# Optimization experiments

Hardware: AMD Instinct MI355X
Metric: run time of the kernel (lower is better)

## Reference

```python
import jax, jax.numpy as jnp
import numpy as np

B, T_EN, T_DE, D_EN, D_DE, UNITS = 8, 512, 128, 512, 512, 256


def setup_inputs() -> dict:
    key = jax.random.key(0)
    k1, k2, k3, k4, k5, k6 = jax.random.split(key, 6)
    return {
        "en_seq": jax.random.normal(k1, (B, T_EN, D_EN), dtype=jnp.float32),
        "de_seq": jax.random.normal(k2, (B, T_DE, D_DE), dtype=jnp.float32),
        "mask_en": jax.random.randint(k3, (B, T_EN), 0, 2, dtype=jnp.int32),
        "w_en": jax.random.normal(k4, (D_EN, UNITS), dtype=jnp.float32) * (1.0 / np.sqrt(D_EN)),
        "w_de": jax.random.normal(k5, (D_DE, UNITS), dtype=jnp.float32) * (1.0 / np.sqrt(D_DE)),
        "nu": jax.random.normal(k6, (UNITS, 1), dtype=jnp.float32) * (1.0 / np.sqrt(UNITS)),
    }


def reference(en_seq, de_seq, mask_en, w_en, w_de, nu):
    # Additive (Bahdanau) attention scores.
    att_en = jnp.einsum('bed,du->beu', en_seq, w_en)   # [B, T_en, U]
    att_de = jnp.einsum('btd,du->btu', de_seq, w_de)   # [B, T_de, U]
    # co_m[b, j, i, u] = att_de[b, j, u] + att_en[b, i, u]
    co_m = jnp.tanh(att_de[:, :, None, :] + att_en[:, None, :, :])  # [B, T_de, T_en, U]
    mu = jnp.einsum('btiu,uo->bti', co_m, nu)          # [B, T_de, T_en]
    # mask: (m - 1) * 1e6 added to logits (m in {0,1})
    m = mask_en.astype(mu.dtype)                       # [B, T_en]
    mu = mu + ((m - 1.0) * 1000000.0)[:, None, :]
    return jax.nn.softmax(mu, axis=-1)                 # [B, T_de, T_en]
```

## Files before the change

### kernel.cpp

```cpp
#include <hip/hip_runtime.h>
#include <cstddef>
#include <cstdint>

#define B_    8
#define T_EN_ 512
#define T_DE_ 128
#define D_    512
#define U_    256

#define TANH_C 2.8853900817779268f
#define L2E_   1.4426950408889634f

typedef float f32x4 __attribute__((ext_vector_type(4)));
typedef float f32x2 __attribute__((ext_vector_type(2)));
typedef short s16x8 __attribute__((ext_vector_type(8)));

__device__ __forceinline__ float exp2c(float x) {
  return __builtin_amdgcn_exp2f(x * TANH_C);
}

__device__ __forceinline__ void split_bf16(float x, short& hi, short& lo) {
  const unsigned u = __float_as_uint(x);
  hi = (short)(u >> 16);
  const float hf = __uint_as_float(u & 0xffff0000u);
  const float lf = x - hf;
  lo = (short)(__float_as_uint(lf) >> 16);
}

__global__ __launch_bounds__(256) void prepack_kernel(
    const float* __restrict__ en, const float* __restrict__ de,
    const float* __restrict__ w_en, const float* __restrict__ w_de,
    short* __restrict__ en_hi, short* __restrict__ en_lo,
    short* __restrict__ de_hi, short* __restrict__ de_lo,
    short* __restrict__ wen_hi, short* __restrict__ wen_lo,
    short* __restrict__ wde_hi, short* __restrict__ wde_lo) {
  const int blk = blockIdx.x;
  const int tid = threadIdx.x;
  float v[8];
  short* ph;
  short* pl;
  size_t ub;

  if (blk < 1280) {
    const int gu = blk * 256 + tid;
    const int n = gu & 15;
    const int g = (gu >> 4) & 3;
    const int s = (gu >> 6) & 15;
    const int rb = gu >> 10;
    const float* src;
    if (rb < 256) {
      const int b = rb >> 5, t = rb & 31;
      src = en + ((size_t)rb * 16 + n) * D_;
      ub = ((size_t)((b * 16 + s) * 32 + t) * 4 + g) * 16 + n;
      ph = en_hi; pl = en_lo;
    } else {
      const int t64 = rb - 256;
      src = de + ((size_t)t64 * 16 + n) * D_;
      ub = ((size_t)(s * 64 + t64) * 4 + g) * 16 + n;
      ph = de_hi; pl = de_lo;
    }
    const int kb = s * 32 + g * 4;
    const float4 fa = *(const float4*)(src + kb);
    const float4 fb = *(const float4*)(src + kb + 16);
    v[0] = fa.x; v[1] = fa.y; v[2] = fa.z; v[3] = fa.w;
    v[4] = fb.x; v[5] = fb.y; v[6] = fb.z; v[7] = fb.w;
  } else {
    const int wb = blk - 1280;
    const bool is_en = wb < 64;
    const int wq = wb & 63;
    const int s = wq >> 2, USq = wq & 3;
    const int n = tid & 15;
    const int g = (tid >> 4) & 3;
    const int US = USq * 4 + (tid >> 6);
    const float* W = is_en ? w_en : w_de;
    ph = is_en ? wen_hi : wde_hi;
    pl = is_en ? wen_lo : wde_lo;
    #pragma unroll
    for (int e = 0; e < 8; ++e) {
      const int k = s * 32 + g * 4 + (e & 3) + 16 * (e >> 2);
      v[e] = W[(size_t)k * U_ + US * 16 + n];
    }
    ub = ((size_t)(s * 16 + US) * 4 + g) * 16 + n;
  }

  s16x8 h8, l8;
  #pragma unroll
  for (int e = 0; e < 8; ++e) {
    short h, l;
    split_bf16(v[e], h, l);
    h8[e] = h; l8[e] = l;
  }
  *(s16x8*)(ph + ub * 8) = h8;
  *(s16x8*)(pl + ub * 8) = l8;
}

__global__ __launch_bounds__(256) void mfma_proj_kernel(
    const short* __restrict__ en_hi, const short* __restrict__ en_lo,
    const short* __restrict__ de_hi, const short* __restrict__ de_lo,
    const short* __restrict__ wen_hi, const short* __restrict__ wen_lo,
    const short* __restrict__ wde_hi, const short* __restrict__ wde_lo,
    float* __restrict__ Et, float* __restrict__ de_t) {
  const int blk = blockIdx.x;
  const int tid = threadIdx.x;
  const int lane = tid & 63;
  const int wv = tid >> 6;
  const int rl = lane >> 4, cl = lane & 15;

  f32x4 acc[2] = {};
  s16x8 bufA[6], bufB[6];

  if (blk < 512) {
    const int b  = blk & 7;
    const int uh = (blk >> 3) & 1;
    const int it = blk >> 4;
    const int US0 = uh * 8 + wv * 2;

#define LOAD_EN(DST, S)                                                   \
    { const size_t oa0 = ((size_t)((S) * 16 + US0) * 64 + lane) * 8;      \
      const size_t ob  = ((size_t)((b * 16 + (S)) * 32 + it) * 64 + lane) * 8; \
      DST[0] = *(const s16x8*)(wen_hi + oa0);                             \
      DST[1] = *(const s16x8*)(wen_lo + oa0);                             \
      DST[2] = *(const s16x8*)(wen_hi + oa0 + 512);                       \
      DST[3] = *(const s16x8*)(wen_lo + oa0 + 512);                       \
      DST[4] = *(const s16x8*)(en_hi + ob);                               \
      DST[5] = *(const s16x8*)(en_lo + ob); }
#define MFMA_EN(S)                                                        \
    { acc[0] = __builtin_amdgcn_mfma_f32_16x16x32_bf16(S[0], S[4], acc[0], 0, 0, 0); \
      acc[0] = __builtin_amdgcn_mfma_f32_16x16x32_bf16(S[0], S[5], acc[0], 0, 0, 0); \
      acc[0] = __builtin_amdgcn_mfma_f32_16x16x32_bf16(S[1], S[4], acc[0], 0, 0, 0); \
      acc[1] = __builtin_amdgcn_mfma_f32_16x16x32_bf16(S[2], S[4], acc[1], 0, 0, 0); \
      acc[1] = __builtin_amdgcn_mfma_f32_16x16x32_bf16(S[2], S[5], acc[1], 0, 0, 0); \
      acc[1] = __builtin_amdgcn_mfma_f32_16x16x32_bf16(S[3], S[4], acc[1], 0, 0, 0); }

    LOAD_EN(bufA, 0)
    for (int s = 0; s < 16; s += 2) {
      LOAD_EN(bufB, s + 1)
      MFMA_EN(bufA)
      if (s + 2 < 16) LOAD_EN(bufA, s + 2)
      MFMA_EN(bufB)
    }
#undef LOAD_EN
#undef MFMA_EN

    #pragma unroll
    for (int us = 0; us < 2; ++us) {
      #pragma unroll
      for (int r = 0; r < 4; ++r) {
        const int u = (US0 + us) * 16 + rl * 4 + r;
        const int i = it * 16 + cl;
        Et[((size_t)b * U_ + u) * T_EN_ + i] = exp2c(acc[us][r]);
      }
    }
  } else {
    const int y = blk - 512;
    const int t64 = y >> 1;
    const int uh = y & 1;
    const int US0 = uh * 8 + wv * 2;

#define LOAD_DE(DST, S)                                                   \
    { const size_t oa = ((size_t)((S) * 64 + t64) * 64 + lane) * 8;       \
      const size_t ob = ((size_t)((S) * 16 + US0) * 64 + lane) * 8;       \
      DST[0] = *(const s16x8*)(de_hi + oa);                               \
      DST[1] = *(const s16x8*)(de_lo + oa);                               \
      DST[2] = *(const s16x8*)(wde_hi + ob);                              \
      DST[3] = *(const s16x8*)(wde_lo + ob);                              \
      DST[4] = *(const s16x8*)(wde_hi + ob + 512);                        \
      DST[5] = *(const s16x8*)(wde_lo + ob + 512); }
#define MFMA_DE(S)                                                        \
    { acc[0] = __builtin_amdgcn_mfma_f32_16x16x32_bf16(S[0], S[2], acc[0], 0, 0, 0); \
      acc[0] = __builtin_amdgcn_mfma_f32_16x16x32_bf16(S[0], S[3], acc[0], 0, 0, 0); \
      acc[0] = __builtin_amdgcn_mfma_f32_16x16x32_bf16(S[1], S[2], acc[0], 0, 0, 0); \
      acc[1] = __builtin_amdgcn_mfma_f32_16x16x32_bf16(S[0], S[4], acc[1], 0, 0, 0); \
      acc[1] = __builtin_amdgcn_mfma_f32_16x16x32_bf16(S[0], S[5], acc[1], 0, 0, 0); \
      acc[1] = __builtin_amdgcn_mfma_f32_16x16x32_bf16(S[1], S[4], acc[1], 0, 0, 0); }

    LOAD_DE(bufA, 0)
    for (int s = 0; s < 16; s += 2) {
      LOAD_DE(bufB, s + 1)
      MFMA_DE(bufA)
      if (s + 2 < 16) LOAD_DE(bufA, s + 2)
      MFMA_DE(bufB)
    }
#undef LOAD_DE
#undef MFMA_DE

    #pragma unroll
    for (int us = 0; us < 2; ++us) {
      #pragma unroll
      for (int r = 0; r < 4; ++r) {
        const int j = t64 * 16 + rl * 4 + r;
        const int u = (US0 + us) * 16 + cl;
        de_t[(size_t)j * U_ + u] = exp2c(acc[us][r]);
      }
    }
  }
}

__global__ __launch_bounds__(512) void attn_mu_softmax_kernel(
    const float* __restrict__ Et, const float* __restrict__ de_t,
    const float* __restrict__ nu, const int* __restrict__ mask,
    float* __restrict__ out) {
  __shared__ f32x2 Ea_s[4][U_ / 2];
  __shared__ f32x2 nv2_s[U_ / 2];
  __shared__ float mu_p[8][4][T_EN_];

  const int tid  = threadIdx.x;
  const int lane = tid & 63;
  const int w    = tid >> 6;
  const int b    = blockIdx.x & 7;
  const int jg   = blockIdx.x >> 3;
  const int j0   = jg * 4;

  {
    const int jl = tid >> 7;
    const int p  = tid & 127;
    const float2 Av = *(const float2*)(de_t + (size_t)(b * T_DE_ + j0 + jl) * U_ + 2 * p);
    f32x2 L; L[0] = Av.x; L[1] = Av.y;
    Ea_s[jl][p] = L;
    if (tid < 128) {
      const float2 n2 = *(const float2*)(nu + 2 * tid);
      f32x2 v; v[0] = n2.x; v[1] = n2.y;
      nv2_s[tid] = v;
    }
  }
  __syncthreads();

  const int pb = w * 16;
  const float* __restrict__ EbA =
      Et + ((size_t)b * U_ + 2 * pb) * T_EN_ + lane * 4;

  const f32x4 one4 = {1.f, 1.f, 1.f, 1.f};
  f32x4 accA[4] = {}, accB[4] = {};

  f32x4 E1Aa, E1Ba, E2Aa, E2Ba, E1Ab, E1Bb, E2Ab, E2Bb;
  f32x2 La[4], Lb[4];
  f32x2 nva, nvb;

#define LOADP(SUF, P)                                                     \
  { const float* e1 = EbA + (size_t)(2 * (P)) * T_EN_;                    \
    const float* e2 = e1 + T_EN_;                                         \
    E1A##SUF = *(const f32x4*)(e1);                                       \
    E1B##SUF = *(const f32x4*)(e1 + 256);                                 \
    E2A##SUF = *(const f32x4*)(e2);                                       \
    E2B##SUF = *(const f32x4*)(e2 + 256);                                 \
    L##SUF[0] = Ea_s[0][pb + (P)];                                        \
    L##SUF[1] = Ea_s[1][pb + (P)];                                        \
    L##SUF[2] = Ea_s[2][pb + (P)];                                        \
    L##SUF[3] = Ea_s[3][pb + (P)];                                        \
    nv##SUF = nv2_s[pb + (P)]; }

#define COMPP(SUF)                                                        \
  { _Pragma("unroll")                                                     \
    for (int jl = 0; jl < 4; ++jl) {                                      \
      const f32x2 Lc = L##SUF[jl];                                        \
      { const f32x4 d1 = E1A##SUF * Lc[0] + one4;                         \
        const f32x4 d2 = E2A##SUF * Lc[1] + one4;                         \
        const f32x4 t  = d2 * nv##SUF[0];                                 \
        const f32x4 num = d1 * nv##SUF[1] + t;                            \
        const f32x4 Dd = d1 * d2;                                         \
        f32x4 r;                                                          \
        r[0] = __builtin_amdgcn_rcpf(Dd[0]);                              \
        r[1] = __builtin_amdgcn_rcpf(Dd[1]);                              \
        r[2] = __builtin_amdgcn_rcpf(Dd[2]);                              \
        r[3] = __builtin_amdgcn_rcpf(Dd[3]);                              \
        accA[jl] = num * r + accA[jl]; }                                  \
      { const f32x4 d1 = E1B##SUF * Lc[0] + one4;                         \
        const f32x4 d2 = E2B##SUF * Lc[1] + one4;                         \
        const f32x4 t  = d2 * nv##SUF[0];                                 \
        const f32x4 num = d1 * nv##SUF[1] + t;                            \
        const f32x4 Dd = d1 * d2;                                         \
        f32x4 r;                                                          \
        r[0] = __builtin_amdgcn_rcpf(Dd[0]);                              \
        r[1] = __builtin_amdgcn_rcpf(Dd[1]);                              \
        r[2] = __builtin_amdgcn_rcpf(Dd[2]);                              \
        r[3] = __builtin_amdgcn_rcpf(Dd[3]);                              \
        accB[jl] = num * r + accB[jl]; }                                  \
    } }

  LOADP(a, 0)
  for (int p0 = 0; p0 < 16; p0 += 2) {
    LOADP(b, p0 + 1)
    COMPP(a)
    if (p0 + 2 < 16) LOADP(a, p0 + 2)
    COMPP(b)
  }
#undef LOADP
#undef COMPP

  #pragma unroll
  for (int jl = 0; jl < 4; ++jl) {
    *(f32x4*)&mu_p[w][jl][lane * 4] = accA[jl];
    *(f32x4*)&mu_p[w][jl][256 + lane * 4] = accB[jl];
  }
  __syncthreads();

  if (w < 4) {
    float vals[8];
    float mx = -3.0e38f;
    #pragma unroll
    for (int h = 0; h < 2; ++h) {
      f32x4 s = {0.f, 0.f, 0.f, 0.f};
      #pragma unroll
      for (int uo = 0; uo < 8; ++uo)
        s += *(const f32x4*)&mu_p[uo][w][h * 256 + lane * 4];
      const int4 mk = *(const int4*)(mask + b * T_EN_ + h * 256 + lane * 4);
      const float v0 = fmaf((float)mk.x - 1.f, 1.0e6f, -2.f * s[0]);
      const float v1 = fmaf((float)mk.y - 1.f, 1.0e6f, -2.f * s[1]);
      const float v2 = fmaf((float)mk.z - 1.f, 1.0e6f, -2.f * s[2]);
      const float v3 = fmaf((float)mk.w - 1.f, 1.0e6f, -2.f * s[3]);
      vals[h * 4 + 0] = v0; vals[h * 4 + 1] = v1;
      vals[h * 4 + 2] = v2; vals[h * 4 + 3] = v3;
      mx = fmaxf(mx, fmaxf(fmaxf(v0, v1), fmaxf(v2, v3)));
    }
    #pragma unroll
    for (int off = 32; off; off >>= 1) mx = fmaxf(mx, __shfl_xor(mx, off, 64));
    float sum = 0.0f;
    #pragma unroll
    for (int k = 0; k < 8; ++k) {
      const float e = __builtin_amdgcn_exp2f((vals[k] - mx) * L2E_);
      vals[k] = e;
      sum += e;
    }
    #pragma unroll
    for (int off = 32; off; off >>= 1) sum += __shfl_xor(sum, off, 64);
    const float inv = __builtin_amdgcn_rcpf(sum);
    float* op = out + (size_t)(b * T_DE_ + j0 + w) * T_EN_;
    #pragma unroll
    for (int h = 0; h < 2; ++h) {
      const float4 o = make_float4(vals[h * 4 + 0] * inv, vals[h * 4 + 1] * inv,
                                   vals[h * 4 + 2] * inv, vals[h * 4 + 3] * inv);
      *(float4*)(op + h * 256 + lane * 4) = o;
    }
  }
}

extern "C" void kernel_launch(void* const* d_in, const int* in_sizes, int n_in,
                              void* d_out, int out_size, void* d_ws, size_t ws_size,
                              hipStream_t stream) {
  const float* en   = (const float*)d_in[0];
  const float* de   = (const float*)d_in[1];
  const int*   mask = (const int*)d_in[2];
  const float* w_en = (const float*)d_in[3];
  const float* w_de = (const float*)d_in[4];
  const float* nu   = (const float*)d_in[5];
  float* out = (float*)d_out;

  float* Et   = (float*)d_ws;
  float* de_t = Et + (size_t)B_ * U_ * T_EN_;
  short* p    = (short*)(de_t + (size_t)B_ * T_DE_ * U_);
  short* en_hi = p;                 p += 2097152;
  short* en_lo = p;                 p += 2097152;
  short* de_hi = p;                 p += 524288;
  short* de_lo = p;                 p += 524288;
  short* wen_hi = p;                p += 131072;
  short* wen_lo = p;                p += 131072;
  short* wde_hi = p;                p += 131072;
  short* wde_lo = p;                p += 131072;

  prepack_kernel<<<dim3(1408), 256, 0, stream>>>(
      en, de, w_en, w_de, en_hi, en_lo, de_hi, de_lo,
      wen_hi, wen_lo, wde_hi, wde_lo);
  mfma_proj_kernel<<<dim3(640), 256, 0, stream>>>(
      en_hi, en_lo, de_hi, de_lo, wen_hi, wen_lo, wde_hi, wde_lo, Et, de_t);
  attn_mu_softmax_kernel<<<dim3(256), 512, 0, stream>>>(
      Et, de_t, nu, mask, out);
}
```

Before: 39.00 us.

## Retile encoder projection and attention kernel; split softmax into separate kernel

The encoder projection now computes two 16-wide i-tiles per wave, reusing each weight fragment across both and halving that part of the grid. The attention kernel now handles 8 decoder rows over half of T_en per block instead of 4 rows over all of T_en, so each Et load is reused across more rows. Because a block no longer sees a full row, softmax moves to a new kernel that reads mu from a workspace buffer. This adds a launch and a global round trip for mu, in exchange for more register-level reuse and better load balance.

```diff
diff --git a/kernel.cpp b/kernel.cpp
--- a/kernel.cpp
+++ b/kernel.cpp
@@ -106,31 +106,39 @@
   const int wv = tid >> 6;
   const int rl = lane >> 4, cl = lane & 15;
 
-  f32x4 acc[2] = {};
-  s16x8 bufA[6], bufB[6];
-
-  if (blk < 512) {
+  if (blk < 256) {
     const int b  = blk & 7;
     const int uh = (blk >> 3) & 1;
     const int it = blk >> 4;
     const int US0 = uh * 8 + wv * 2;
 
+    f32x4 acc[2][2] = {};
+    s16x8 bufA[8], bufB[8];
+
 #define LOAD_EN(DST, S)                                                   \
     { const size_t oa0 = ((size_t)((S) * 16 + US0) * 64 + lane) * 8;      \
-      const size_t ob  = ((size_t)((b * 16 + (S)) * 32 + it) * 64 + lane) * 8; \
+      const size_t ob0 = ((size_t)(((b * 16 + (S)) * 32 + it * 2)) * 64 + lane) * 8; \
       DST[0] = *(const s16x8*)(wen_hi + oa0);                             \
       DST[1] = *(const s16x8*)(wen_lo + oa0);                             \
       DST[2] = *(const s16x8*)(wen_hi + oa0 + 512);                       \
       DST[3] = *(const s16x8*)(wen_lo + oa0 + 512);                       \
-      DST[4] = *(const s16x8*)(en_hi + ob);                               \
-      DST[5] = *(const s16x8*)(en_lo + ob); }
+      DST[4] = *(const s16x8*)(en_hi + ob0);                              \
+      DST[5] = *(const s16x8*)(en_lo + ob0);                              \
+      DST[6] = *(const s16x8*)(en_hi + ob0 + 512);                        \
+      DST[7] = *(const s16x8*)(en_lo + ob0 + 512); }
 #define MFMA_EN(S)                                                        \
-    { acc[0] = __builtin_amdgcn_mfma_f32_16x16x32_bf16(S[0], S[4], acc[0], 0, 0, 0); \
-      acc[0] = __builtin_amdgcn_mfma_f32_16x16x32_bf16(S[0], S[5], acc[0], 0, 0, 0); \
-      acc[0] = __builtin_amdgcn_mfma_f32_16x16x32_bf16(S[1], S[4], acc[0], 0, 0, 0); \
-      acc[1] = __builtin_amdgcn_mfma_f32_16x16x32_bf16(S[2], S[4], acc[1], 0, 0, 0); \
-      acc[1] = __builtin_amdgcn_mfma_f32_16x16x32_bf16(S[2], S[5], acc[1], 0, 0, 0); \
-      acc[1] = __builtin_amdgcn_mfma_f32_16x16x32_bf16(S[3], S[4], acc[1], 0, 0, 0); }
+    { acc[0][0] = __builtin_amdgcn_mfma_f32_16x16x32_bf16(S[0], S[4], acc[0][0], 0, 0, 0); \
+      acc[0][0] = __builtin_amdgcn_mfma_f32_16x16x32_bf16(S[0], S[5], acc[0][0], 0, 0, 0); \
+      acc[0][0] = __builtin_amdgcn_mfma_f32_16x16x32_bf16(S[1], S[4], acc[0][0], 0, 0, 0); \
+      acc[0][1] = __builtin_amdgcn_mfma_f32_16x16x32_bf16(S[0], S[6], acc[0][1], 0, 0, 0); \
+      acc[0][1] = __builtin_amdgcn_mfma_f32_16x16x32_bf16(S[0], S[7], acc[0][1], 0, 0, 0); \
+      acc[0][1] = __builtin_amdgcn_mfma_f32_16x16x32_bf16(S[1], S[6], acc[0][1], 0, 0, 0); \
+      acc[1][0] = __builtin_amdgcn_mfma_f32_16x16x32_bf16(S[2], S[4], acc[1][0], 0, 0, 0); \
+      acc[1][0] = __builtin_amdgcn_mfma_f32_16x16x32_bf16(S[2], S[5], acc[1][0], 0, 0, 0); \
+      acc[1][0] = __builtin_amdgcn_mfma_f32_16x16x32_bf16(S[3], S[4], acc[1][0], 0, 0, 0); \
+      acc[1][1] = __builtin_amdgcn_mfma_f32_16x16x32_bf16(S[2], S[6], acc[1][1], 0, 0, 0); \
+      acc[1][1] = __builtin_amdgcn_mfma_f32_16x16x32_bf16(S[2], S[7], acc[1][1], 0, 0, 0); \
+      acc[1][1] = __builtin_amdgcn_mfma_f32_16x16x32_bf16(S[3], S[6], acc[1][1], 0, 0, 0); }
 
     LOAD_EN(bufA, 0)
     for (int s = 0; s < 16; s += 2) {
@@ -145,17 +153,23 @@
     #pragma unroll
     for (int us = 0; us < 2; ++us) {
       #pragma unroll
-      for (int r = 0; r < 4; ++r) {
-        const int u = (US0 + us) * 16 + rl * 4 + r;
-        const int i = it * 16 + cl;
-        Et[((size_t)b * U_ + u) * T_EN_ + i] = exp2c(acc[us][r]);
+      for (int is = 0; is < 2; ++is) {
+        #pragma unroll
+        for (int r = 0; r < 4; ++r) {
+          const int u = (US0 + us) * 16 + rl * 4 + r;
+          const int i = it * 32 + is * 16 + cl;
+          Et[((size_t)b * U_ + u) * T_EN_ + i] = exp2c(acc[us][is][r]);
+        }
       }
     }
   } else {
-    const int y = blk - 512;
+    const int y = blk - 256;
     const int t64 = y >> 1;
     const int uh = y & 1;
     const int US0 = uh * 8 + wv * 2;
+
+    f32x4 acc[2] = {};
+    s16x8 bufA[6], bufB[6];
 
 #define LOAD_DE(DST, S)                                                   \
     { const size_t oa = ((size_t)((S) * 64 + t64) * 64 + lane) * 8;       \
@@ -196,85 +210,71 @@
   }
 }
 
-__global__ __launch_bounds__(512) void attn_mu_softmax_kernel(
+__global__ __launch_bounds__(512) void attn_mu_kernel(
     const float* __restrict__ Et, const float* __restrict__ de_t,
-    const float* __restrict__ nu, const int* __restrict__ mask,
-    float* __restrict__ out) {
-  __shared__ f32x2 Ea_s[4][U_ / 2];
+    const float* __restrict__ nu, float* __restrict__ mu) {
+  __shared__ f32x2 Ea_s[8][U_ / 2];
   __shared__ f32x2 nv2_s[U_ / 2];
-  __shared__ float mu_p[8][4][T_EN_];
+  __shared__ float mu_p[8][8][256];
 
   const int tid  = threadIdx.x;
   const int lane = tid & 63;
   const int w    = tid >> 6;
   const int b    = blockIdx.x & 7;
-  const int jg   = blockIdx.x >> 3;
-  const int j0   = jg * 4;
-
-  {
-    const int jl = tid >> 7;
-    const int p  = tid & 127;
+  const int ih   = (blockIdx.x >> 3) & 1;
+  const int jo   = blockIdx.x >> 4;
+  const int j0   = jo * 8;
+
+  #pragma unroll
+  for (int e0 = 0; e0 < 2; ++e0) {
+    const int e = tid + e0 * 512;
+    const int jl = e >> 7;
+    const int p  = e & 127;
     const float2 Av = *(const float2*)(de_t + (size_t)(b * T_DE_ + j0 + jl) * U_ + 2 * p);
     f32x2 L; L[0] = Av.x; L[1] = Av.y;
     Ea_s[jl][p] = L;
-    if (tid < 128) {
-      const float2 n2 = *(const float2*)(nu + 2 * tid);
-      f32x2 v; v[0] = n2.x; v[1] = n2.y;
-      nv2_s[tid] = v;
-    }
+  }
+  if (tid < 128) {
+    const float2 n2 = *(const float2*)(nu + 2 * tid);
+    f32x2 v; v[0] = n2.x; v[1] = n2.y;
+    nv2_s[tid] = v;
   }
   __syncthreads();
 
   const int pb = w * 16;
-  const float* __restrict__ EbA =
-      Et + ((size_t)b * U_ + 2 * pb) * T_EN_ + lane * 4;
+  const float* __restrict__ Eb =
+      Et + ((size_t)b * U_ + 2 * pb) * T_EN_ + ih * 256 + lane * 4;
 
   const f32x4 one4 = {1.f, 1.f, 1.f, 1.f};
-  f32x4 accA[4] = {}, accB[4] = {};
-
-  f32x4 E1Aa, E1Ba, E2Aa, E2Ba, E1Ab, E1Bb, E2Ab, E2Bb;
-  f32x2 La[4], Lb[4];
+  f32x4 acc[8] = {};
+
+  f32x4 E1a, E2a, E1b, E2b;
+  f32x2 La[8], Lb[8];
   f32x2 nva, nvb;
 
 #define LOADP(SUF, P)                                                     \
-  { const float* e1 = EbA + (size_t)(2 * (P)) * T_EN_;                    \
-    const float* e2 = e1 + T_EN_;                                         \
-    E1A##SUF = *(const f32x4*)(e1);                                       \
-    E1B##SUF = *(const f32x4*)(e1 + 256);                                 \
-    E2A##SUF = *(const f32x4*)(e2);                                       \
-    E2B##SUF = *(const f32x4*)(e2 + 256);                                 \
-    L##SUF[0] = Ea_s[0][pb + (P)];                                        \
-    L##SUF[1] = Ea_s[1][pb + (P)];                                        \
-    L##SUF[2] = Ea_s[2][pb + (P)];                                        \
-    L##SUF[3] = Ea_s[3][pb + (P)];                                        \
+  { const float* e1 = Eb + (size_t)(2 * (P)) * T_EN_;                     \
+    E1##SUF = *(const f32x4*)(e1);                                        \
+    E2##SUF = *(const f32x4*)(e1 + T_EN_);                                \
+    _Pragma("unroll")                                                     \
+    for (int jl = 0; jl < 8; ++jl) L##SUF[jl] = Ea_s[jl][pb + (P)];       \
     nv##SUF = nv2_s[pb + (P)]; }
 
 #define COMPP(SUF)                                                        \
   { _Pragma("unroll")                                                     \
-    for (int jl = 0; jl < 4; ++jl) {                                      \
+    for (int jl = 0; jl < 8; ++jl) {                                      \
       const f32x2 Lc = L##SUF[jl];                                        \
-      { const f32x4 d1 = E1A##SUF * Lc[0] + one4;                         \
-        const f32x4 d2 = E2A##SUF * Lc[1] + one4;                         \
-        const f32x4 t  = d2 * nv##SUF[0];                                 \
-        const f32x4 num = d1 * nv##SUF[1] + t;                            \
-        const f32x4 Dd = d1 * d2;                                         \
-        f32x4 r;                                                          \
-        r[0] = __builtin_amdgcn_rcpf(Dd[0]);                              \
-        r[1] = __builtin_amdgcn_rcpf(Dd[1]);                              \
-        r[2] = __builtin_amdgcn_rcpf(Dd[2]);                              \
-        r[3] = __builtin_amdgcn_rcpf(Dd[3]);                              \
-        accA[jl] = num * r + accA[jl]; }                                  \
-      { const f32x4 d1 = E1B##SUF * Lc[0] + one4;                         \
-        const f32x4 d2 = E2B##SUF * Lc[1] + one4;                         \
-        const f32x4 t  = d2 * nv##SUF[0];                                 \
-        const f32x4 num = d1 * nv##SUF[1] + t;                            \
-        const f32x4 Dd = d1 * d2;                                         \
-        f32x4 r;                                                          \
-        r[0] = __builtin_amdgcn_rcpf(Dd[0]);                              \
-        r[1] = __builtin_amdgcn_rcpf(Dd[1]);                              \
-        r[2] = __builtin_amdgcn_rcpf(Dd[2]);                              \
-        r[3] = __builtin_amdgcn_rcpf(Dd[3]);                              \
-        accB[jl] = num * r + accB[jl]; }                                  \
+      const f32x4 d1 = E1##SUF * Lc[0] + one4;                            \
+      const f32x4 d2 = E2##SUF * Lc[1] + one4;                            \
+      const f32x4 t  = d2 * nv##SUF[0];                                   \
+      const f32x4 num = d1 * nv##SUF[1] + t;                              \
+      const f32x4 Dd = d1 * d2;                                           \
+      f32x4 r;                                                            \
+      r[0] = __builtin_amdgcn_rcpf(Dd[0]);                                \
+      r[1] = __builtin_amdgcn_rcpf(Dd[1]);                                \
+      r[2] = __builtin_amdgcn_rcpf(Dd[2]);                                \
+      r[3] = __builtin_amdgcn_rcpf(Dd[3]);                                \
+      acc[jl] = num * r + acc[jl];                                        \
     } }
 
   LOADP(a, 0)
@@ -288,50 +288,54 @@
 #undef COMPP
 
   #pragma unroll
-  for (int jl = 0; jl < 4; ++jl) {
-    *(f32x4*)&mu_p[w][jl][lane * 4] = accA[jl];
-    *(f32x4*)&mu_p[w][jl][256 + lane * 4] = accB[jl];
-  }
+  for (int jl = 0; jl < 8; ++jl)
+    *(f32x4*)&mu_p[w][jl][lane * 4] = acc[jl];
   __syncthreads();
 
-  if (w < 4) {
-    float vals[8];
-    float mx = -3.0e38f;
+  {
+    f32x4 s = {0.f, 0.f, 0.f, 0.f};
     #pragma unroll
-    for (int h = 0; h < 2; ++h) {
-      f32x4 s = {0.f, 0.f, 0.f, 0.f};
-      #pragma unroll
-      for (int uo = 0; uo < 8; ++uo)
-        s += *(const f32x4*)&mu_p[uo][w][h * 256 + lane * 4];
-      const int4 mk = *(const int4*)(mask + b * T_EN_ + h * 256 + lane * 4);
-      const float v0 = fmaf((float)mk.x - 1.f, 1.0e6f, -2.f * s[0]);
-      const float v1 = fmaf((float)mk.y - 1.f, 1.0e6f, -2.f * s[1]);
-      const float v2 = fmaf((float)mk.z - 1.f, 1.0e6f, -2.f * s[2]);
-      const float v3 = fmaf((float)mk.w - 1.f, 1.0e6f, -2.f * s[3]);
-      vals[h * 4 + 0] = v0; vals[h * 4 + 1] = v1;
-      vals[h * 4 + 2] = v2; vals[h * 4 + 3] = v3;
-      mx = fmaxf(mx, fmaxf(fmaxf(v0, v1), fmaxf(v2, v3)));
-    }
-    #pragma unroll
-    for (int off = 32; off; off >>= 1) mx = fmaxf(mx, __shfl_xor(mx, off, 64));
-    float sum = 0.0f;
-    #pragma unroll
-    for (int k = 0; k < 8; ++k) {
-      const float e = __builtin_amdgcn_exp2f((vals[k] - mx) * L2E_);
-      vals[k] = e;
-      sum += e;
-    }
-    #pragma unroll
-    for (int off = 32; off; off >>= 1) sum += __shfl_xor(sum, off, 64);
-    const float inv = __builtin_amdgcn_rcpf(sum);
-    float* op = out + (size_t)(b * T_DE_ + j0 + w) * T_EN_;
-    #pragma unroll
-    for (int h = 0; h < 2; ++h) {
-      const float4 o = make_float4(vals[h * 4 + 0] * inv, vals[h * 4 + 1] * inv,
-                                   vals[h * 4 + 2] * inv, vals[h * 4 + 3] * inv);
-      *(float4*)(op + h * 256 + lane * 4) = o;
-    }
-  }
+    for (int uo = 0; uo < 8; ++uo)
+      s += *(const f32x4*)&mu_p[uo][w][lane * 4];
+    const f32x4 o = s * -2.0f;
+    *(f32x4*)(mu + (size_t)(b * T_DE_ + j0 + w) * T_EN_ + ih * 256 + lane * 4) = o;
+  }
+}
+
+__global__ __launch_bounds__(512) void softmax_kernel(
+    const float* __restrict__ mu, const int* __restrict__ mask,
+    float* __restrict__ out) {
+  const int tid  = threadIdx.x;
+  const int lane = tid & 63;
+  const int jd   = blockIdx.x * 8 + (tid >> 6);
+  const int b    = jd >> 7;
+
+  const float* mp = mu + (size_t)jd * T_EN_;
+  float vals[8];
+  float mx = -3.0e38f;
+  #pragma unroll
+  for (int k = 0; k < 8; ++k) {
+    const int i = lane + 64 * k;
+    const float mi = (float)mask[b * T_EN_ + i];
+    const float v = fmaf(mi - 1.0f, 1.0e6f, mp[i]);
+    vals[k] = v;
+    mx = fmaxf(mx, v);
+  }
+  #pragma unroll
+  for (int off = 32; off; off >>= 1) mx = fmaxf(mx, __shfl_xor(mx, off, 64));
+  float sum = 0.0f;
+  #pragma unroll
+  for (int k = 0; k < 8; ++k) {
+    const float e = __builtin_amdgcn_exp2f((vals[k] - mx) * L2E_);
+    vals[k] = e;
+    sum += e;
+  }
+  #pragma unroll
+  for (int off = 32; off; off >>= 1) sum += __shfl_xor(sum, off, 64);
+  const float inv = __builtin_amdgcn_rcpf(sum);
+  float* op = out + (size_t)jd * T_EN_;
+  #pragma unroll
+  for (int k = 0; k < 8; ++k) op[lane + 64 * k] = vals[k] * inv;
 }
 
 extern "C" void kernel_launch(void* const* d_in, const int* in_sizes, int n_in,
@@ -347,7 +351,8 @@
 
   float* Et   = (float*)d_ws;
   float* de_t = Et + (size_t)B_ * U_ * T_EN_;
-  short* p    = (short*)(de_t + (size_t)B_ * T_DE_ * U_);
+  float* muB  = de_t + (size_t)B_ * T_DE_ * U_;
+  short* p    = (short*)(muB + (size_t)B_ * T_DE_ * T_EN_);
   short* en_hi = p;                 p += 2097152;
   short* en_lo = p;                 p += 2097152;
   short* de_hi = p;                 p += 524288;
@@ -360,8 +365,8 @@
   prepack_kernel<<<dim3(1408), 256, 0, stream>>>(
       en, de, w_en, w_de, en_hi, en_lo, de_hi, de_lo,
       wen_hi, wen_lo, wde_hi, wde_lo);
-  mfma_proj_kernel<<<dim3(640), 256, 0, stream>>>(
+  mfma_proj_kernel<<<dim3(384), 256, 0, stream>>>(
       en_hi, en_lo, de_hi, de_lo, wen_hi, wen_lo, wde_hi, wde_lo, Et, de_t);
-  attn_mu_softmax_kernel<<<dim3(256), 512, 0, stream>>>(
-      Et, de_t, nu, mask, out);
-}
+  attn_mu_kernel<<<dim3(256), 512, 0, stream>>>(Et, de_t, nu, muB);
+  softmax_kernel<<<dim3(128), 512, 0, stream>>>(muB, mask, out);
+}
```

Result: slower. 41.11 us (+5.4%).

## Deepen projection load prefetch and halve decoder rows per attention block

Applied to the files above, without the earlier changes.

The projection kernel now keeps four stages of register buffers in flight instead of two, aiming to hide more global load latency behind the MFMAs. The attention kernel handles 2 decoder rows per block instead of 4, doubling the grid to 512 blocks, shrinking shared memory, and adding a min-blocks hint to raise occupancy. The trade-off is that each Et tile loaded from global memory is now reused across fewer decoder rows, doubling Et traffic. The extra prefetch buffers also raise register pressure.

```diff
diff --git a/kernel.cpp b/kernel.cpp
--- a/kernel.cpp
+++ b/kernel.cpp
@@ -107,7 +107,7 @@
   const int rl = lane >> 4, cl = lane & 15;
 
   f32x4 acc[2] = {};
-  s16x8 bufA[6], bufB[6];
+  s16x8 bA[6], bB[6], bC[6], bD[6];
 
   if (blk < 512) {
     const int b  = blk & 7;
@@ -132,12 +132,20 @@
       acc[1] = __builtin_amdgcn_mfma_f32_16x16x32_bf16(S[2], S[5], acc[1], 0, 0, 0); \
       acc[1] = __builtin_amdgcn_mfma_f32_16x16x32_bf16(S[3], S[4], acc[1], 0, 0, 0); }
 
-    LOAD_EN(bufA, 0)
-    for (int s = 0; s < 16; s += 2) {
-      LOAD_EN(bufB, s + 1)
-      MFMA_EN(bufA)
-      if (s + 2 < 16) LOAD_EN(bufA, s + 2)
-      MFMA_EN(bufB)
+    LOAD_EN(bA, 0)
+    LOAD_EN(bB, 1)
+    LOAD_EN(bC, 2)
+    LOAD_EN(bD, 3)
+    #pragma unroll
+    for (int s = 0; s < 16; s += 4) {
+      MFMA_EN(bA)
+      if (s + 4 < 16) LOAD_EN(bA, s + 4)
+      MFMA_EN(bB)
+      if (s + 5 < 16) LOAD_EN(bB, s + 5)
+      MFMA_EN(bC)
+      if (s + 6 < 16) LOAD_EN(bC, s + 6)
+      MFMA_EN(bD)
+      if (s + 7 < 16) LOAD_EN(bD, s + 7)
     }
 #undef LOAD_EN
 #undef MFMA_EN
@@ -174,12 +182,20 @@
       acc[1] = __builtin_amdgcn_mfma_f32_16x16x32_bf16(S[0], S[5], acc[1], 0, 0, 0); \
       acc[1] = __builtin_amdgcn_mfma_f32_16x16x32_bf16(S[1], S[4], acc[1], 0, 0, 0); }
 
-    LOAD_DE(bufA, 0)
-    for (int s = 0; s < 16; s += 2) {
-      LOAD_DE(bufB, s + 1)
-      MFMA_DE(bufA)
-      if (s + 2 < 16) LOAD_DE(bufA, s + 2)
-      MFMA_DE(bufB)
+    LOAD_DE(bA, 0)
+    LOAD_DE(bB, 1)
+    LOAD_DE(bC, 2)
+    LOAD_DE(bD, 3)
+    #pragma unroll
+    for (int s = 0; s < 16; s += 4) {
+      MFMA_DE(bA)
+      if (s + 4 < 16) LOAD_DE(bA, s + 4)
+      MFMA_DE(bB)
+      if (s + 5 < 16) LOAD_DE(bB, s + 5)
+      MFMA_DE(bC)
+      if (s + 6 < 16) LOAD_DE(bC, s + 6)
+      MFMA_DE(bD)
+      if (s + 7 < 16) LOAD_DE(bD, s + 7)
     }
 #undef LOAD_DE
 #undef MFMA_DE
@@ -196,32 +212,32 @@
   }
 }
 
-__global__ __launch_bounds__(512) void attn_mu_softmax_kernel(
+__global__ __launch_bounds__(512, 4) void attn_mu_softmax_kernel(
     const float* __restrict__ Et, const float* __restrict__ de_t,
     const float* __restrict__ nu, const int* __restrict__ mask,
     float* __restrict__ out) {
-  __shared__ f32x2 Ea_s[4][U_ / 2];
+  __shared__ f32x2 Ea_s[2][U_ / 2];
   __shared__ f32x2 nv2_s[U_ / 2];
-  __shared__ float mu_p[8][4][T_EN_];
+  __shared__ float mu_p[8][2][T_EN_];
 
   const int tid  = threadIdx.x;
   const int lane = tid & 63;
   const int w    = tid >> 6;
   const int b    = blockIdx.x & 7;
-  const int jg   = blockIdx.x >> 3;
-  const int j0   = jg * 4;
-
-  {
+  const int jp   = blockIdx.x >> 3;
+  const int j0   = jp * 2;
+
+  if (tid < 256) {
     const int jl = tid >> 7;
     const int p  = tid & 127;
     const float2 Av = *(const float2*)(de_t + (size_t)(b * T_DE_ + j0 + jl) * U_ + 2 * p);
     f32x2 L; L[0] = Av.x; L[1] = Av.y;
     Ea_s[jl][p] = L;
-    if (tid < 128) {
-      const float2 n2 = *(const float2*)(nu + 2 * tid);
-      f32x2 v; v[0] = n2.x; v[1] = n2.y;
-      nv2_s[tid] = v;
-    }
+  }
+  if (tid < 128) {
+    const float2 n2 = *(const float2*)(nu + 2 * tid);
+    f32x2 v; v[0] = n2.x; v[1] = n2.y;
+    nv2_s[tid] = v;
   }
   __syncthreads();
 
@@ -230,10 +246,10 @@
       Et + ((size_t)b * U_ + 2 * pb) * T_EN_ + lane * 4;
 
   const f32x4 one4 = {1.f, 1.f, 1.f, 1.f};
-  f32x4 accA[4] = {}, accB[4] = {};
+  f32x4 accA[2] = {}, accB[2] = {};
 
   f32x4 E1Aa, E1Ba, E2Aa, E2Ba, E1Ab, E1Bb, E2Ab, E2Bb;
-  f32x2 La[4], Lb[4];
+  f32x2 La[2], Lb[2];
   f32x2 nva, nvb;
 
 #define LOADP(SUF, P)                                                     \
@@ -245,13 +261,11 @@
     E2B##SUF = *(const f32x4*)(e2 + 256);                                 \
     L##SUF[0] = Ea_s[0][pb + (P)];                                        \
     L##SUF[1] = Ea_s[1][pb + (P)];                                        \
-    L##SUF[2] = Ea_s[2][pb + (P)];                                        \
-    L##SUF[3] = Ea_s[3][pb + (P)];                                        \
     nv##SUF = nv2_s[pb + (P)]; }
 
 #define COMPP(SUF)                                                        \
   { _Pragma("unroll")                                                     \
-    for (int jl = 0; jl < 4; ++jl) {                                      \
+    for (int jl = 0; jl < 2; ++jl) {                                      \
       const f32x2 Lc = L##SUF[jl];                                        \
       { const f32x4 d1 = E1A##SUF * Lc[0] + one4;                         \
         const f32x4 d2 = E2A##SUF * Lc[1] + one4;                         \
@@ -288,13 +302,13 @@
 #undef COMPP
 
   #pragma unroll
-  for (int jl = 0; jl < 4; ++jl) {
+  for (int jl = 0; jl < 2; ++jl) {
     *(f32x4*)&mu_p[w][jl][lane * 4] = accA[jl];
     *(f32x4*)&mu_p[w][jl][256 + lane * 4] = accB[jl];
   }
   __syncthreads();
 
-  if (w < 4) {
+  if (w < 2) {
     float vals[8];
     float mx = -3.0e38f;
     #pragma unroll
@@ -362,6 +376,6 @@
       wen_hi, wen_lo, wde_hi, wde_lo);
   mfma_proj_kernel<<<dim3(640), 256, 0, stream>>>(
       en_hi, en_lo, de_hi, de_lo, wen_hi, wen_lo, wde_hi, wde_lo, Et, de_t);
-  attn_mu_softmax_kernel<<<dim3(256), 512, 0, stream>>>(
+  attn_mu_softmax_kernel<<<dim3(512), 512, 0, stream>>>(
       Et, de_t, nu, mask, out);
 }
```

Result: no change. 39.24 us (+0.6%).
